# Kernel tuning notes

Measured on AMD Instinct MI355X. Metric: run time of the kernel, lower is better.

## Reference

```python
import jax, jax.numpy as jnp
import numpy as np
import math

H_HEADS = 4
SQRT_2_PI = math.sqrt(2.0 / math.pi)


def _gelu_tanh(x):
    return 0.5 * x * (1.0 + jnp.tanh(SQRT_2_PI * (x + 0.044715 * x ** 3)))


def _ln(x, g, b, eps=1e-5):
    mu = jnp.mean(x, axis=-1, keepdims=True)
    var = jnp.var(x, axis=-1, keepdims=True)
    return g * (x - mu) * jax.lax.rsqrt(var + eps) + b


def _forward(support_emb_mat, query_t, support_t, cls_embed, t_freq, t_phase,
             Wq, bq, Wk, bk, Wv, bv, Wo, bo, ln1_g, ln1_b, time_w,
             W1, b1, W2, b2, ln2_g, ln2_b, Wc, bc, bn_g, bn_b):
    B, F, MD = support_emb_mat.shape
    Q = query_t.shape[1]
    S = F + 1
    H = H_HEADS
    D = MD * H
    dph = D // H
    L = Wq.shape[0]
    BQ = B * Q

    # [CLS] + support sequence, feature-tiled to model_dim*num_heads
    cls = jnp.broadcast_to(cls_embed, (B, 1, MD))
    seq = jnp.concatenate([cls, support_emb_mat], axis=1)          # [B,S,MD]
    x = jnp.tile(seq, (1, 1, H))                                    # [B,S,D]
    x = jnp.broadcast_to(x[:, None], (B, Q, S, D)).reshape(BQ, S, D)

    # time sequence: [query_t_q, support_t...] per (b,q)
    sup = jnp.broadcast_to(support_t[:, None, :], (B, Q, F))
    t_seq = jnp.concatenate([query_t[..., None], sup], axis=-1).reshape(BQ, S)
    t_diff = t_seq[:, :, None] - t_seq[:, None, :]                  # [BQ,S,S]
    # time encoder: cos(t*freq + phase) -> [BQ,S,S,TD]
    t_emb = jnp.cos(t_diff[..., None] * t_freq + t_phase)

    # scale as in source: (dim_per_head // num_heads) ** -0.5
    scale = (dph // H) ** (-0.5)

    for l in range(L):
        bias = t_emb @ time_w[l]                                    # [BQ,S,S]
        add = jnp.tile(bias, (H, 1, 1))                             # [BQ*H,S,S]
        res = x
        # raw row-major reshape to (BQ*H, S, dph) exactly as torch .view
        q = (x @ Wq[l] + bq[l]).reshape(BQ * H, S, dph)
        k = (x @ Wk[l] + bk[l]).reshape(BQ * H, S, dph)
        v = (x @ Wv[l] + bv[l]).reshape(BQ * H, S, dph)
        attn = jax.nn.softmax(jnp.einsum('bsd,btd->bst', q, k) * scale + add, axis=-1)
        ctx = jnp.einsum('bst,btd->bsd', attn, v).reshape(BQ, S, D)
        out = _ln(res + ctx @ Wo[l] + bo[l], ln1_g[l], ln1_b[l])
        ffn = _gelu_tanh(out @ W1[l] + b1[l]) @ W2[l] + b2[l]
        x = _ln(out + ffn, ln2_g[l], ln2_b[l])

    # compress: Linear -> BatchNorm1d over seq channels (train mode) -> LeakyReLU
    h = x @ Wc + bc                                                 # [BQ,S,MD]
    mu = jnp.mean(h, axis=(0, 2), keepdims=True)
    var = jnp.var(h, axis=(0, 2), keepdims=True)
    h = bn_g[None, :, None] * (h - mu) * jax.lax.rsqrt(var + 1e-5) + bn_b[None, :, None]
    h = jnp.where(h >= 0, h, 0.01 * h)                              # LeakyReLU
    return h[:, 0, :].reshape(B, Q, MD)


def setup_inputs() -> dict:
    key = jax.random.key(0)
    ks = jax.random.split(key, 24)
    B, Q, F, MD = 128, 32, 7, 128
    H, L, FFN, TD = 4, 6, 2048, 32
    S = F + 1
    D = MD * H

    def nrm(k, shape, s=0.02):
        return jax.random.normal(k, shape, jnp.float32) * s

    inp = {
        'support_emb_mat': jax.random.normal(ks[0], (B, F, MD), jnp.float32),
        'query_t': jax.random.uniform(ks[1], (B, Q), jnp.float32) * 100.0,
        'support_t': jax.random.uniform(ks[2], (B, F), jnp.float32) * 100.0,
        'cls_embed': jax.random.uniform(ks[3], (1, MD), jnp.float32),
        't_freq': nrm(ks[4], (TD,), 1.0),
        't_phase': nrm(ks[5], (TD,), 1.0),
        'Wq': nrm(ks[6], (L, D, D)), 'bq': jnp.zeros((L, D)),
        'Wk': nrm(ks[7], (L, D, D)), 'bk': jnp.zeros((L, D)),
        'Wv': nrm(ks[8], (L, D, D)), 'bv': jnp.zeros((L, D)),
        'Wo': nrm(ks[9], (L, D, D)), 'bo': jnp.zeros((L, D)),
        'ln1_g': jnp.ones((L, D)), 'ln1_b': jnp.zeros((L, D)),
        'time_w': jnp.ones((L, TD)) * 0.001,
        'W1': nrm(ks[10], (L, D, FFN)), 'b1': jnp.zeros((L, FFN)),
        'W2': nrm(ks[11], (L, FFN, D)), 'b2': jnp.zeros((L, D)),
        'ln2_g': jnp.ones((L, D)), 'ln2_b': jnp.zeros((L, D)),
        'Wc': nrm(ks[12], (D, MD)), 'bc': jnp.zeros((MD,)),
        'bn_g': jnp.ones((S,)), 'bn_b': jnp.zeros((S,)),
    }
    return inp


def reference(support_emb_mat, query_t, support_t, cls_embed, t_freq, t_phase,
              Wq, bq, Wk, bk, Wv, bv, Wo, bo, ln1_g, ln1_b, time_w,
              W1, b1, W2, b2, ln2_g, ln2_b, Wc, bc, bn_g, bn_b):
    return _forward(support_emb_mat, query_t, support_t, cls_embed, t_freq, t_phase,
                    Wq, bq, Wk, bk, Wv, bv, Wo, bo, ln1_g, ln1_b, time_w,
                    W1, b1, W2, b2, ln2_g, ln2_b, Wc, bc, bn_g, bn_b)
```

## Files before the change

kernel.cpp:

```cpp
#include <hip/hip_runtime.h>
#include <hip/hip_bf16.h>

typedef _Float16 f16;
typedef __attribute__((ext_vector_type(8))) _Float16 f16x8;
typedef __attribute__((ext_vector_type(4))) _Float16 f16x4;
typedef __attribute__((ext_vector_type(4))) float f32x4;

#define DEVI __device__ __forceinline__

DEVI float ldf(const void* p, size_t i, int isf32) {
    if (isf32) return ((const float*)p)[i];
    unsigned int u = ((const unsigned short*)p)[i];
    union { unsigned int b; float f; } c; c.b = u << 16;
    return c.f;
}

DEVI void gld_lds16(const f16* g, f16* l) {
    __builtin_amdgcn_global_load_lds(
        (__attribute__((address_space(1))) void*)(g),
        (__attribute__((address_space(3))) void*)(l), 16, 0, 0);
}

__global__ void detect_dtype(const void* qt, int* flag) {
    if (threadIdx.x == 0 && blockIdx.x == 0) {
        const unsigned int* w = (const unsigned int*)qt;
        int cnt = 0;
        for (int i = 0; i < 64; ++i) {
            unsigned int lo = w[i] & 0xFFFFu;
            union { unsigned int b; float f; } c; c.b = lo << 16;
            if (c.f >= 1e-4f && c.f <= 100.5f) ++cnt;
        }
        *flag = (cnt >= 32) ? 0 : 1;
    }
}

__global__ __launch_bounds__(256)
void cvt_in(const void* __restrict__ src, float* __restrict__ dst, int n,
            const int* __restrict__ flag) {
    const int f32 = *flag;
    int i = blockIdx.x * 256 + threadIdx.x;
    if (i < n) dst[i] = ldf(src, i, f32);
}

__global__ __launch_bounds__(256)
void fill_out(float* out, float v) {
    out[blockIdx.x * 256 + threadIdx.x] = v;
}

template<int EPI>
__global__ __launch_bounds__(256, 4)
void gemm_bt(const f16* __restrict__ Ag, const f16* __restrict__ BTg,
             const float* __restrict__ biasg, const f16* __restrict__ resg,
             void* __restrict__ outg,
             int NT, int NTZ, int MCHUNK, int MT, int N, int K, int lda,
             long zsB, long zsBias, long zsC)
{
    const int tid  = threadIdx.x;
    const int w    = tid >> 6, lane = tid & 63;
    const int wm   = w >> 1,   wn   = w & 1;

    const int id    = blockIdx.x;
    const int pc    = MCHUNK * NTZ;
    const int chunk = id / pc;
    const int rem   = id - chunk * pc;
    const int mloc  = rem % MCHUNK;
    const int ynz   = rem / MCHUNK;
    const int z     = ynz / NT;
    const int tmB   = (chunk * MCHUNK + mloc) * (128 * MT);
    const int tn    = (ynz - z * NT) * 128;

    const f16*   BT   = BTg + (size_t)z * zsB;
    const float* bias = biasg + (size_t)z * zsBias;
    const size_t zoffC = (size_t)z * zsC;

    __shared__ __align__(16) f16 smA[2][8][64][8];
    __shared__ __align__(16) f16 smB[2][8][64][8];

    const int r16 = lane & 15, q4 = lane >> 4;
    const int iters = K >> 5;

    const f16* gA0 = Ag + (size_t)(tmB + (2 * w) * 16 + r16) * lda + q4 * 8;
    const f16* gA1 = gA0 + (size_t)16 * lda;
    const f16* gB0 = BT + (size_t)(tn + (2 * w) * 16 + r16) * K + q4 * 8;
    const f16* gB1 = gB0 + (size_t)16 * K;

    auto issue = [&](int msN, int ktN, int buf) {
        const size_t aoff = (size_t)msN * 128 * lda + (size_t)ktN * 32;
        const size_t boff = (size_t)ktN * 32;
        gld_lds16(gA0 + aoff, &smA[buf][2 * w][0][0]);
        gld_lds16(gA1 + aoff, &smA[buf][2 * w + 1][0][0]);
        gld_lds16(gB0 + boff, &smB[buf][2 * w][0][0]);
        gld_lds16(gB1 + boff, &smB[buf][2 * w + 1][0][0]);
    };

    issue(0, 0, 0);
    int stage = 0;

    for (int ms = 0; ms < MT; ++ms) {
        const int tm = tmB + ms * 128;

        f32x4 acc[4][4];
#pragma unroll
        for (int i = 0; i < 4; ++i)
#pragma unroll
            for (int j = 0; j < 4; ++j) acc[i][j] = (f32x4)0.0f;

        for (int kt = 0; kt < iters; ++kt, ++stage) {
            const int cur = stage & 1;
            __builtin_amdgcn_s_barrier();
            int ktN = kt + 1, msN = ms;
            if (ktN == iters) { ktN = 0; ++msN; }
            if (msN < MT) {
                issue(msN, ktN, cur ^ 1);
                __builtin_amdgcn_s_waitcnt(0x0F74);
            } else {
                __builtin_amdgcn_s_waitcnt(0x0F70);
            }
            __builtin_amdgcn_s_barrier();
            __asm__ __volatile__("" ::: "memory");

            f16x8 af[4], bf[4];
#pragma unroll
            for (int i = 0; i < 4; ++i) {
                af[i] = *(const f16x8*)&smA[cur][wm * 4 + i][lane][0];
                bf[i] = *(const f16x8*)&smB[cur][wn * 4 + i][lane][0];
            }
#pragma unroll
            for (int i = 0; i < 4; ++i)
#pragma unroll
                for (int j = 0; j < 4; ++j)
                    acc[i][j] = __builtin_amdgcn_mfma_f32_16x16x32_f16(
                        bf[j], af[i], acc[i][j], 0, 0, 0);
        }

        const int rowBase = tm + wm * 64;
        const int colBase = tn + wn * 64;
#pragma unroll
        for (int i = 0; i < 4; ++i) {
            const int row = rowBase + i * 16 + r16;
            const size_t rowoff = (size_t)row * N;
#pragma unroll
            for (int j = 0; j < 4; ++j) {
                const int n0 = colBase + j * 16 + q4 * 4;
                const f32x4 bv4 = *(const f32x4*)&bias[n0];
                if constexpr (EPI == 3) {
                    f32x4 o;
#pragma unroll
                    for (int r = 0; r < 4; ++r) o[r] = acc[i][j][r] + bv4[r];
                    *(f32x4*)((float*)outg + rowoff + n0) = o;
                } else {
                    f16x4 o;
#pragma unroll
                    for (int r = 0; r < 4; ++r) {
                        float v = acc[i][j][r] + bv4[r];
                        if constexpr (EPI == 2) {
                            float v2 = v * v;
                            float t  = v * (1.0f + 0.044715f * v2);
                            float e  = __expf(1.5957691216057308f * t);
                            float rc = __builtin_amdgcn_rcpf(e + 1.0f);
                            v = v - v * rc;
                        }
                        o[r] = (f16)v;
                    }
                    *(f16x4*)((f16*)outg + zoffC + rowoff + n0) = o;
                }
            }
        }
    }
}

__global__ __launch_bounds__(512, 2)
void gemm_ln(const f16* __restrict__ Ag, const f16* __restrict__ BTg,
             const float* __restrict__ bias, const f16* __restrict__ resg,
             const float* __restrict__ lng, const float* __restrict__ lnb,
             f16* __restrict__ Yg, int K, int lda)
{
    const int tid = threadIdx.x;
    const int w = tid >> 6, lane = tid & 63;
    const int wm = w >> 2, wn = w & 3;
    const int r16 = lane & 15, q4 = lane >> 4;
    const int tm = blockIdx.x * 128;

    __shared__ __align__(16) f16 smA[2][8][64][8];
    __shared__ __align__(16) f16 smB[2][32][64][8];
    __shared__ __align__(16) float lnS[128][4];
    __shared__ __align__(16) float lnQ[128][4];

    f32x4 acc[4][8];
#pragma unroll
    for (int i = 0; i < 4; ++i)
#pragma unroll
        for (int j = 0; j < 8; ++j) acc[i][j] = (f32x4)0.0f;

    const f16* gA  = Ag  + (size_t)(tm + w * 16 + r16) * lda + q4 * 8;
    const f16* gB  = BTg + (size_t)(w * 64 + r16) * K + q4 * 8;
    const int iters = K >> 5;

    auto issue = [&](int kt, int buf) {
        const size_t o = (size_t)kt * 32;
        gld_lds16(gA + o, &smA[buf][w][0][0]);
#pragma unroll
        for (int t = 0; t < 4; ++t)
            gld_lds16(gB + (size_t)(t * 16) * K + o, &smB[buf][w * 4 + t][0][0]);
    };

    issue(0, 0);
    for (int kt = 0; kt < iters; ++kt) {
        const int cur = kt & 1;
        __builtin_amdgcn_s_barrier();
        if (kt + 1 < iters) {
            issue(kt + 1, cur ^ 1);
            __builtin_amdgcn_s_waitcnt(0x0F75);
        } else {
            __builtin_amdgcn_s_waitcnt(0x0F70);
        }
        __builtin_amdgcn_s_barrier();
        __asm__ __volatile__("" ::: "memory");

        f16x8 af[4], bf[8];
#pragma unroll
        for (int i = 0; i < 4; ++i)
            af[i] = *(const f16x8*)&smA[cur][wm * 4 + i][lane][0];
#pragma unroll
        for (int j = 0; j < 8; ++j)
            bf[j] = *(const f16x8*)&smB[cur][wn * 8 + j][lane][0];
#pragma unroll
        for (int i = 0; i < 4; ++i)
#pragma unroll
            for (int j = 0; j < 8; ++j)
                acc[i][j] = __builtin_amdgcn_mfma_f32_16x16x32_f16(
                    bf[j], af[i], acc[i][j], 0, 0, 0);
    }

    const int rowB = wm * 64;
    const int colB = wn * 128;

    float ps[4], pq[4];
#pragma unroll
    for (int i = 0; i < 4; ++i) {
        const int grow = tm + rowB + i * 16 + r16;
        const size_t roff = (size_t)grow * 512;
        float s = 0.f, sq = 0.f;
#pragma unroll
        for (int j = 0; j < 8; ++j) {
            const int n0 = colB + j * 16 + q4 * 4;
            const f32x4 biv = *(const f32x4*)&bias[n0];
            const f16x4 rv  = *(const f16x4*)&resg[roff + n0];
#pragma unroll
            for (int r = 0; r < 4; ++r) {
                float v = acc[i][j][r] + biv[r] + (float)rv[r];
                acc[i][j][r] = v;
                s += v; sq += v * v;
            }
        }
        s  += __shfl_xor(s, 16, 64);  s  += __shfl_xor(s, 32, 64);
        sq += __shfl_xor(sq, 16, 64); sq += __shfl_xor(sq, 32, 64);
        ps[i] = s; pq[i] = sq;
    }
    if (q4 == 0) {
#pragma unroll
        for (int i = 0; i < 4; ++i) {
            const int lr = rowB + i * 16 + r16;
            lnS[lr][wn] = ps[i];
            lnQ[lr][wn] = pq[i];
        }
    }
    __syncthreads();

#pragma unroll
    for (int i = 0; i < 4; ++i) {
        const int lr = rowB + i * 16 + r16;
        const f32x4 s4 = *(const f32x4*)&lnS[lr][0];
        const f32x4 q4v = *(const f32x4*)&lnQ[lr][0];
        const float s  = s4[0] + s4[1] + s4[2] + s4[3];
        const float sq = q4v[0] + q4v[1] + q4v[2] + q4v[3];
        const float mu = s * (1.0f / 512.0f);
        const float var = sq * (1.0f / 512.0f) - mu * mu;
        const float rs = rsqrtf(var + 1e-5f);
        const size_t rowoff = (size_t)(tm + lr) * 512;
#pragma unroll
        for (int j = 0; j < 8; ++j) {
            const int n0 = colB + j * 16 + q4 * 4;
            const f32x4 g4 = *(const f32x4*)&lng[n0];
            const f32x4 b4 = *(const f32x4*)&lnb[n0];
            f16x4 o;
#pragma unroll
            for (int r = 0; r < 4; ++r)
                o[r] = (f16)(g4[r] * (acc[i][j][r] - mu) * rs + b4[r]);
            *(f16x4*)&Yg[rowoff + n0] = o;
        }
    }
}

__global__ __launch_bounds__(256)
void attn_kernel(const f16* __restrict__ qg, const f16* __restrict__ kg,
                 const f16* __restrict__ vg, const float* __restrict__ biasL,
                 f16* __restrict__ cg, int small)
{
    const int w = threadIdx.x >> 6, lane = threadIdx.x & 63;
    const int j = blockIdx.x * 4 + w;
    __shared__ __align__(16) f16 sQ[4][8][136];
    __shared__ __align__(16) f16 sK[4][8][136];
    __shared__ __align__(16) f16 sV[4][8][136];
    __shared__ float sP[4][8][8];

    const size_t base  = (size_t)j * 1024;
    const size_t ibase = small ? ((size_t)(j >> 7) * 4096 + (size_t)(j & 3) * 1024)
                               : base;
#pragma unroll
    for (int t = 0; t < 2; ++t) {
        int flat = (t * 64 + lane) * 8;
        int r = flat >> 7, c = flat & 127;
        *(f16x8*)&sQ[w][r][c] = *(const f16x8*)(qg + ibase + flat);
        *(f16x8*)&sK[w][r][c] = *(const f16x8*)(kg + ibase + flat);
        *(f16x8*)&sV[w][r][c] = *(const f16x8*)(vg + ibase + flat);
    }
    __syncthreads();

    const int i = lane >> 3, jj = lane & 7;
    float d = 0.f;
#pragma unroll
    for (int c = 0; c < 16; ++c) {
        f16x8 qv = *(const f16x8*)&sQ[w][i][c * 8];
        f16x8 kv = *(const f16x8*)&sK[w][jj][c * 8];
#pragma unroll
        for (int e = 0; e < 8; ++e) d += (float)qv[e] * (float)kv[e];
    }
    float s = d * 0.17677669529663687f + biasL[(size_t)(j & 4095) * 64 + lane];
    float mx = s;
    mx = fmaxf(mx, __shfl_xor(mx, 1, 64));
    mx = fmaxf(mx, __shfl_xor(mx, 2, 64));
    mx = fmaxf(mx, __shfl_xor(mx, 4, 64));
    float p = __expf(s - mx);
    float sum = p;
    sum += __shfl_xor(sum, 1, 64);
    sum += __shfl_xor(sum, 2, 64);
    sum += __shfl_xor(sum, 4, 64);
    sP[w][i][jj] = p / sum;
    __syncthreads();

#pragma unroll
    for (int t2 = 0; t2 < 8; ++t2) {
        float ap[8];
#pragma unroll
        for (int e = 0; e < 8; ++e) ap[e] = sP[w][t2][e];
#pragma unroll
        for (int h = 0; h < 2; ++h) {
            int flat = (t2 * 2 + h) * 64 + lane;
            int dd = flat & 127;
            float o = 0.f;
#pragma unroll
            for (int e = 0; e < 8; ++e) o += ap[e] * (float)sV[w][e][dd];
            cg[base + flat] = (f16)o;
        }
    }
}

__global__ __launch_bounds__(256)
void build_x0(const void* __restrict__ sup, const void* __restrict__ cls,
              f16* __restrict__ xb, const int* __restrict__ flag)
{
    const int f32 = *flag;
    const size_t idx = ((size_t)blockIdx.x * 256 + threadIdx.x) * 4;
    const int row = (int)(idx >> 9), col0 = (int)(idx & 511);
    const int s = row & 7, b = row >> 8;
    f16x4 o;
#pragma unroll
    for (int e = 0; e < 4; ++e) {
        const int md = (col0 + e) & 127;
        float v = (s == 0) ? ldf(cls, md, f32)
                           : ldf(sup, ((size_t)b * 7 + (s - 1)) * 128 + md, f32);
        o[e] = (f16)v;
    }
    *(f16x4*)(xb + idx) = o;
}

__global__ __launch_bounds__(256)
void build_x0s(const void* __restrict__ sup, const void* __restrict__ cls,
               f16* __restrict__ xs, const int* __restrict__ flag)
{
    const int f32 = *flag;
    const size_t idx = ((size_t)blockIdx.x * 256 + threadIdx.x) * 4;
    const int row = (int)(idx >> 9), col0 = (int)(idx & 511);
    const int s = row & 7, b = row >> 3;
    f16x4 o;
#pragma unroll
    for (int e = 0; e < 4; ++e) {
        const int md = (col0 + e) & 127;
        float v = (s == 0) ? ldf(cls, md, f32)
                           : ldf(sup, ((size_t)b * 7 + (s - 1)) * 128 + md, f32);
        o[e] = (f16)v;
    }
    *(f16x4*)(xs + idx) = o;
}

__global__ __launch_bounds__(256)
void bias_kernel(const void* __restrict__ qt, const void* __restrict__ st,
                 const void* __restrict__ freq, const void* __restrict__ phase,
                 const void* __restrict__ tw, float* __restrict__ biasAll,
                 const int* __restrict__ flag)
{
    const int f32 = *flag;
    const int lane = threadIdx.x & 63;
    const int bq = blockIdx.x * 4 + (threadIdx.x >> 6);
    const int b = bq >> 5, qq = bq & 31;
    const int i = lane >> 3, jj = lane & 7;
    const float ti = (i  == 0) ? ldf(qt, b * 32 + qq, f32) : ldf(st, b * 7 + i  - 1, f32);
    const float tj = (jj == 0) ? ldf(qt, b * 32 + qq, f32) : ldf(st, b * 7 + jj - 1, f32);
    const float td = ti - tj;
    float a[6] = {0.f, 0.f, 0.f, 0.f, 0.f, 0.f};
    for (int t = 0; t < 32; ++t) {
        float c = __cosf(td * ldf(freq, t, f32) + ldf(phase, t, f32));
#pragma unroll
        for (int l = 0; l < 6; ++l) a[l] += c * ldf(tw, l * 32 + t, f32);
    }
#pragma unroll
    for (int l = 0; l < 6; ++l)
        biasAll[(size_t)l * (4096 * 64) + (size_t)bq * 64 + lane] = a[l];
}

__global__ __launch_bounds__(256)
void transpose_cvt(const void* __restrict__ W, f16* __restrict__ WT,
                   int K, int N, long zsW, long zsWT, const int* __restrict__ flag)
{
    const int f32 = *flag;
    const size_t zoff = (size_t)blockIdx.z * zsW;
    f16* WTz = WT + (size_t)blockIdx.z * zsWT;
    __shared__ float tile[64][65];
    const int tn = blockIdx.x * 64, tk = blockIdx.y * 64;
#pragma unroll
    for (int t = 0; t < 16; ++t) {
        int idx = t * 256 + threadIdx.x;
        int r = idx >> 6, c = idx & 63;
        tile[r][c] = ldf(W, zoff + (size_t)(tk + r) * N + tn + c, f32);
    }
    __syncthreads();
#pragma unroll
    for (int t = 0; t < 16; ++t) {
        int idx = t * 256 + threadIdx.x;
        int r = idx >> 6, c = idx & 63;
        WTz[(size_t)(tn + r) * K + tk + c] = (f16)tile[c][r];
    }
}

__global__ __launch_bounds__(256)
void gather_qkvb(const void* __restrict__ bq, const void* __restrict__ bk,
                 const void* __restrict__ bv, float* __restrict__ dst,
                 const int* __restrict__ flag)
{
    const int f32 = *flag;
    int i = blockIdx.x * 256 + threadIdx.x;
    if (i < 9216) {
        int z = i / 3072, rem = i % 3072;
        const void* src = (z == 0) ? bq : ((z == 1) ? bk : bv);
        dst[i] = ldf(src, rem, f32);
    }
}

__global__ __launch_bounds__(256)
void bn_reduce(const float* __restrict__ h0, float* __restrict__ stats)
{
    const int t = blockIdx.x * 256 + threadIdx.x;
    float s = 0.f, ss = 0.f;
#pragma unroll
    for (int k = 0; k < 8; ++k) {
        float v = h0[t + k * 65536];
        s += v; ss += v * v;
    }
#pragma unroll
    for (int m = 1; m <= 32; m <<= 1) {
        s  += __shfl_xor(s, m, 64);
        ss += __shfl_xor(ss, m, 64);
    }
    __shared__ float ls[8];
    const int w = threadIdx.x >> 6, lane = threadIdx.x & 63;
    if (lane == 0) { ls[w] = s; ls[4 + w] = ss; }
    __syncthreads();
    if (threadIdx.x == 0) {
        atomicAdd(&stats[0], ls[0] + ls[1] + ls[2] + ls[3]);
        atomicAdd(&stats[1], ls[4] + ls[5] + ls[6] + ls[7]);
    }
}

__global__ __launch_bounds__(256)
void bn_apply(const float* __restrict__ h0, const float* __restrict__ stats,
              const float* __restrict__ bnp, float* __restrict__ out)
{
    const int t = blockIdx.x * 256 + threadIdx.x;
    const float mu  = stats[0] * (1.0f / 524288.0f);
    const float var = stats[1] * (1.0f / 524288.0f) - mu * mu;
    const float rs  = rsqrtf(var + 1e-5f);
    float v = bnp[0] * (h0[t] - mu) * rs + bnp[8];
    v = (v >= 0.f) ? v : 0.01f * v;
    out[t] = v;
}

extern "C" void kernel_launch(void* const* d_in, const int* in_sizes, int n_in,
                              void* d_out, int out_size, void* d_ws, size_t ws_size,
                              hipStream_t stream)
{
    (void)in_sizes; (void)n_in; (void)out_size;
    const void* sup   = d_in[0];
    const void* qt    = d_in[1];
    const void* st    = d_in[2];
    const void* cls   = d_in[3];
    const void* freq  = d_in[4];
    const void* phase = d_in[5];
    const void* Wq = d_in[6];  const void* bqv = d_in[7];
    const void* Wk = d_in[8];  const void* bkv = d_in[9];
    const void* Wv = d_in[10]; const void* bvv = d_in[11];
    const void* Wo = d_in[12]; const void* bo  = d_in[13];
    const void* ln1g = d_in[14]; const void* ln1b = d_in[15];
    const void* tw = d_in[16];
    const void* W1 = d_in[17]; const void* b1 = d_in[18];
    const void* W2 = d_in[19]; const void* b2 = d_in[20];
    const void* ln2g = d_in[21]; const void* ln2b = d_in[22];
    const void* Wc = d_in[23]; const void* bc = d_in[24];
    const void* bng = d_in[25]; const void* bnb = d_in[26];

    const size_t NEEDED = 245658240;
    if (ws_size < NEEDED) {
        fill_out<<<2048, 256, 0, stream>>>((float*)d_out, 999.0f);
        return;
    }

    char* ws = (char*)d_ws;
    f16*   wt      = (f16*)(ws + 0);
    float* biasAll = (float*)(ws + 37879808);
    float* qkvb    = (float*)(ws + 44171264);
    float* prm     = (float*)(ws + 44208128);
    float* stats   = (float*)(ws + 44331584);
    int*   flag    = (int*)  (ws + 44331592);
    f16*   xb      = (f16*)(ws + 44331648);
    f16*   ob      = (f16*)(ws + 77886080);
    char*  region  = ws + 111440512;
    f16*   qb      = (f16*)(region);
    f16*   kb      = (f16*)(region + 33554432);
    f16*   vb      = (f16*)(region + 67108864);
    f16*   cb      = (f16*)(region + 100663296);
    f16*   qs      = (f16*)(region);
    f16*   xs      = (f16*)(region + 100663296);
    f16*   fbuf    = (f16*)(region);
    float* h0      = (float*)(region);

    detect_dtype<<<1, 64, 0, stream>>>(qt, flag);

    cvt_in<<<12, 256, 0, stream>>>(bo,   prm + 0,     3072,  flag);
    cvt_in<<<48, 256, 0, stream>>>(b1,   prm + 3072,  12288, flag);
    cvt_in<<<12, 256, 0, stream>>>(b2,   prm + 15360, 3072,  flag);
    cvt_in<<<1,  256, 0, stream>>>(bc,   prm + 18432, 128,   flag);
    cvt_in<<<12, 256, 0, stream>>>(ln1g, prm + 18560, 3072,  flag);
    cvt_in<<<12, 256, 0, stream>>>(ln1b, prm + 21632, 3072,  flag);
    cvt_in<<<12, 256, 0, stream>>>(ln2g, prm + 24704, 3072,  flag);
    cvt_in<<<12, 256, 0, stream>>>(ln2b, prm + 27776, 3072,  flag);
    cvt_in<<<1,  256, 0, stream>>>(bng,  prm + 30848, 8,     flag);
    cvt_in<<<1,  256, 0, stream>>>(bnb,  prm + 30856, 8,     flag);

    transpose_cvt<<<dim3(8, 8, 6),  256, 0, stream>>>(Wq, wt + 0,        512, 512,  262144, 262144, flag);
    transpose_cvt<<<dim3(8, 8, 6),  256, 0, stream>>>(Wk, wt + 1572864,  512, 512,  262144, 262144, flag);
    transpose_cvt<<<dim3(8, 8, 6),  256, 0, stream>>>(Wv, wt + 3145728,  512, 512,  262144, 262144, flag);
    transpose_cvt<<<dim3(8, 8, 6),  256, 0, stream>>>(Wo, wt + 4718592,  512, 512,  262144, 262144, flag);
    transpose_cvt<<<dim3(32, 8, 6), 256, 0, stream>>>(W1, wt + 6291456,  512, 2048, 1048576, 1048576, flag);
    transpose_cvt<<<dim3(8, 32, 6), 256, 0, stream>>>(W2, wt + 12582912, 2048, 512, 1048576, 1048576, flag);
    transpose_cvt<<<dim3(2, 8, 1),  256, 0, stream>>>(Wc, wt + 18874368, 512, 128,  0, 0, flag);
    gather_qkvb<<<36, 256, 0, stream>>>(bqv, bkv, bvv, qkvb, flag);
    build_x0<<<16384, 256, 0, stream>>>(sup, cls, xb, flag);
    build_x0s<<<512, 256, 0, stream>>>(sup, cls, xs, flag);
    bias_kernel<<<1024, 256, 0, stream>>>(qt, st, freq, phase, tw, biasAll, flag);
    hipMemsetAsync(stats, 0, 8, stream);

    for (int l = 0; l < 6; ++l) {
        if (l == 0) {
            gemm_bt<0><<<96, 256, 0, stream>>>(
                xs, wt, qkvb, nullptr, qs,
                4, 12, 8, 1, 512, 512, 512, 1572864, 3072, 524288);
            attn_kernel<<<4096, 256, 0, stream>>>(
                qs, qs + 524288, qs + 1048576, biasAll, cb, 1);
        } else {
            gemm_bt<0><<<1536, 256, 0, stream>>>(
                xb, wt + l * 262144, qkvb + l * 512, nullptr, qb,
                4, 12, 32, 2, 512, 512, 512, 1572864, 3072, 16777216);
            attn_kernel<<<4096, 256, 0, stream>>>(
                qb, kb, vb, biasAll + (size_t)l * 262144, cb, 0);
        }
        gemm_ln<<<256, 512, 0, stream>>>(
            cb, wt + 4718592 + l * 262144, prm + 0 + l * 512, xb,
            prm + 18560 + l * 512, prm + 21632 + l * 512, ob, 512, 512);
        gemm_bt<2><<<2048, 256, 0, stream>>>(
            ob, wt + 6291456 + l * 1048576, prm + 3072 + l * 2048, nullptr, fbuf,
            16, 16, 32, 2, 2048, 512, 512, 0, 0, 0);
        gemm_ln<<<256, 512, 0, stream>>>(
            fbuf, wt + 12582912 + l * 1048576, prm + 15360 + l * 512, ob,
            prm + 24704 + l * 512, prm + 27776 + l * 512, xb, 2048, 2048);
    }

    gemm_bt<3><<<32, 256, 0, stream>>>(
        xb, wt + 18874368, prm + 18432, nullptr, h0,
        1, 1, 32, 1, 128, 512, 4096 , 0, 0, 0);
    bn_reduce<<<256, 256, 0, stream>>>(h0, stats);
    bn_apply<<<2048, 256, 0, stream>>>(h0, stats, prm + 30848, (float*)d_out);
}
```

Measured before the change: 2.911 ms.

## Add 256x256-tile GEMM kernel for QKV and FFN1 projections

Introduces a new 512-thread GEMM with 256x256 output tiles, a 64-wide K step, double-buffered global-to-LDS loads, and an XCD-aware block remapping. It replaces the older gemm_bt for the QKV projections and the GELU FFN-up projection. Larger tiles raise arithmetic intensity and cut redundant operand loads. The cost is higher register and LDS pressure (128 accumulator floats per thread) and fewer blocks, especially the 24-block layer-0 launch.

New measurement: 2.876 ms. About the same (-1.2%).

```diff
diff --git a/kernel.cpp b/kernel.cpp
--- a/kernel.cpp
+++ b/kernel.cpp
@@ -45,6 +45,122 @@
 __global__ __launch_bounds__(256)
 void fill_out(float* out, float v) {
     out[blockIdx.x * 256 + threadIdx.x] = v;
+}
+
+template<int EPI>
+__global__ __launch_bounds__(512, 2)
+void gemm256(const f16* __restrict__ Ag, const f16* __restrict__ BTg,
+             const float* __restrict__ biasg, void* __restrict__ outg,
+             int gridM, int gridN, int N, int K, int lda,
+             long zsB, long zsBias, long zsC)
+{
+    const int tid = threadIdx.x;
+    const int w = tid >> 6, lane = tid & 63;
+    const int wm = w >> 2, wn = w & 3;
+    const int r16 = lane & 15, q4 = lane >> 4;
+
+    const int cpx = gridDim.x >> 3;
+    const int id  = (blockIdx.x & 7) * cpx + (blockIdx.x >> 3);
+
+    const int mloc = id % gridM;
+    const int ynz  = id / gridM;
+    const int z    = ynz / gridN;
+    const int nt   = ynz - z * gridN;
+    const int tm = mloc * 256, tn = nt * 256;
+
+    const f16*   BT   = BTg + (size_t)z * zsB;
+    const float* bias = biasg + (size_t)z * zsBias;
+    const size_t zoffC = (size_t)z * zsC;
+
+    __shared__ __align__(16) f16 smA[2][2][16][64][8];
+    __shared__ __align__(16) f16 smB[2][2][16][64][8];
+
+    const f16* gA[4]; const f16* gB[4];
+#pragma unroll
+    for (int t = 0; t < 4; ++t) {
+        const int c = 4 * w + t, kk = c >> 4, rc = c & 15;
+        gA[t] = Ag + (size_t)(tm + rc * 16 + r16) * lda + kk * 32 + q4 * 8;
+        gB[t] = BT + (size_t)(tn + rc * 16 + r16) * K  + kk * 32 + q4 * 8;
+    }
+    f16* const smAbase = &smA[0][0][0][0][0];
+    f16* const smBbase = &smB[0][0][0][0][0];
+    const int coff = (4 * w) * 512;
+
+    auto issue = [&](int kt, int buf) {
+        const size_t o = (size_t)kt * 64;
+        const int bo = buf * 16384 + coff;
+#pragma unroll
+        for (int t = 0; t < 4; ++t) {
+            gld_lds16(gA[t] + o, smAbase + bo + t * 512);
+            gld_lds16(gB[t] + o, smBbase + bo + t * 512);
+        }
+    };
+
+    f32x4 acc[8][4];
+#pragma unroll
+    for (int i = 0; i < 8; ++i)
+#pragma unroll
+        for (int j = 0; j < 4; ++j) acc[i][j] = (f32x4)0.0f;
+
+    const int iters = K >> 6;
+    issue(0, 0);
+    __builtin_amdgcn_s_waitcnt(0x0F70);
+    __builtin_amdgcn_s_barrier();
+    __asm__ __volatile__("" ::: "memory");
+
+    for (int kt = 0; kt < iters; ++kt) {
+        const int cur = kt & 1;
+        const bool more = (kt + 1 < iters);
+        if (more) issue(kt + 1, cur ^ 1);
+#pragma unroll
+        for (int kk = 0; kk < 2; ++kk) {
+            f16x8 af[8], bf[4];
+#pragma unroll
+            for (int i = 0; i < 8; ++i)
+                af[i] = *(const f16x8*)&smA[cur][kk][wm * 8 + i][lane][0];
+#pragma unroll
+            for (int j = 0; j < 4; ++j)
+                bf[j] = *(const f16x8*)&smB[cur][kk][wn * 4 + j][lane][0];
+#pragma unroll
+            for (int i = 0; i < 8; ++i)
+#pragma unroll
+                for (int j = 0; j < 4; ++j)
+                    acc[i][j] = __builtin_amdgcn_mfma_f32_16x16x32_f16(
+                        bf[j], af[i], acc[i][j], 0, 0, 0);
+        }
+        if (more) {
+            __builtin_amdgcn_s_waitcnt(0x0F70);
+            __builtin_amdgcn_s_barrier();
+            __asm__ __volatile__("" ::: "memory");
+        }
+    }
+
+    const int rowBase = tm + wm * 128;
+    const int colBase = tn + wn * 64;
+#pragma unroll
+    for (int i = 0; i < 8; ++i) {
+        const int row = rowBase + i * 16 + r16;
+        const size_t rowoff = (size_t)row * N;
+#pragma unroll
+        for (int j = 0; j < 4; ++j) {
+            const int n0 = colBase + j * 16 + q4 * 4;
+            const f32x4 bv4 = *(const f32x4*)&bias[n0];
+            f16x4 o;
+#pragma unroll
+            for (int r = 0; r < 4; ++r) {
+                float v = acc[i][j][r] + bv4[r];
+                if constexpr (EPI == 2) {
+                    float v2 = v * v;
+                    float t  = v * (1.0f + 0.044715f * v2);
+                    float e  = __expf(1.5957691216057308f * t);
+                    float rc = __builtin_amdgcn_rcpf(e + 1.0f);
+                    v = v - v * rc;
+                }
+                o[r] = (f16)v;
+            }
+            *(f16x4*)((f16*)outg + zoffC + rowoff + n0) = o;
+        }
+    }
 }
 
 template<int EPI>
@@ -571,24 +687,24 @@
 
     for (int l = 0; l < 6; ++l) {
         if (l == 0) {
-            gemm_bt<0><<<96, 256, 0, stream>>>(
-                xs, wt, qkvb, nullptr, qs,
-                4, 12, 8, 1, 512, 512, 512, 1572864, 3072, 524288);
+            gemm256<0><<<24, 512, 0, stream>>>(
+                xs, wt, qkvb, qs,
+                4, 2, 512, 512, 512, 1572864, 3072, 524288);
             attn_kernel<<<4096, 256, 0, stream>>>(
                 qs, qs + 524288, qs + 1048576, biasAll, cb, 1);
         } else {
-            gemm_bt<0><<<1536, 256, 0, stream>>>(
-                xb, wt + l * 262144, qkvb + l * 512, nullptr, qb,
-                4, 12, 32, 2, 512, 512, 512, 1572864, 3072, 16777216);
+            gemm256<0><<<768, 512, 0, stream>>>(
+                xb, wt + l * 262144, qkvb + l * 512, qb,
+                128, 2, 512, 512, 512, 1572864, 3072, 16777216);
             attn_kernel<<<4096, 256, 0, stream>>>(
                 qb, kb, vb, biasAll + (size_t)l * 262144, cb, 0);
         }
         gemm_ln<<<256, 512, 0, stream>>>(
             cb, wt + 4718592 + l * 262144, prm + 0 + l * 512, xb,
             prm + 18560 + l * 512, prm + 21632 + l * 512, ob, 512, 512);
-        gemm_bt<2><<<2048, 256, 0, stream>>>(
-            ob, wt + 6291456 + l * 1048576, prm + 3072 + l * 2048, nullptr, fbuf,
-            16, 16, 32, 2, 2048, 512, 512, 0, 0, 0);
+        gemm256<2><<<1024, 512, 0, stream>>>(
+            ob, wt + 6291456 + l * 1048576, prm + 3072 + l * 2048, fbuf,
+            128, 8, 2048, 512, 512, 0, 0, 0);
         gemm_ln<<<256, 512, 0, stream>>>(
             fbuf, wt + 12582912 + l * 1048576, prm + 15360 + l * 512, ob,
             prm + 24704 + l * 512, prm + 27776 + l * 512, xb, 2048, 2048);
```

## Compute last-layer FFN only for CLS rows and simplify GEMM tiling

Applied to the files above, without the earlier changes.

Replaces the multi-M-tile gemm_bt with a simpler one-tile-per-block kernel that uses an XCD-aware block index swizzle. It also restricts the final layer's FFN and its LayerNorm to only the rows the classifier reads (stride 4096, i.e. the CLS rows), which drops most of the last FFN's work. The cost is more blocks, with the prologue repeated per tile, and no cross-M-tile prefetch.

After: 2.830 ms. -2.8%, faster.

```diff
diff --git a/kernel.cpp b/kernel.cpp
--- a/kernel.cpp
+++ b/kernel.cpp
@@ -49,25 +49,24 @@
 
 template<int EPI>
 __global__ __launch_bounds__(256, 4)
-void gemm_bt(const f16* __restrict__ Ag, const f16* __restrict__ BTg,
-             const float* __restrict__ biasg, const f16* __restrict__ resg,
-             void* __restrict__ outg,
-             int NT, int NTZ, int MCHUNK, int MT, int N, int K, int lda,
-             long zsB, long zsBias, long zsC)
+void gemm_bt2(const f16* __restrict__ Ag, const f16* __restrict__ BTg,
+              const float* __restrict__ biasg, void* __restrict__ outg,
+              int NZ, int gridN, int N, int K, int lda,
+              long zsB, long zsBias, long zsC)
 {
     const int tid  = threadIdx.x;
     const int w    = tid >> 6, lane = tid & 63;
     const int wm   = w >> 1,   wn   = w & 1;
-
-    const int id    = blockIdx.x;
-    const int pc    = MCHUNK * NTZ;
-    const int chunk = id / pc;
-    const int rem   = id - chunk * pc;
-    const int mloc  = rem % MCHUNK;
-    const int ynz   = rem / MCHUNK;
-    const int z     = ynz / NT;
-    const int tmB   = (chunk * MCHUNK + mloc) * (128 * MT);
-    const int tn    = (ynz - z * NT) * 128;
+    const int r16  = lane & 15, q4 = lane >> 4;
+
+    const int cpx = gridDim.x >> 3;
+    const int id  = (blockIdx.x & 7) * cpx + (blockIdx.x >> 3);
+
+    const int nz   = id % NZ;
+    const int mloc = id / NZ;
+    const int z    = nz / gridN;
+    const int nt   = nz - z * gridN;
+    const int tm   = mloc * 128, tn = nt * 128;
 
     const f16*   BT   = BTg + (size_t)z * zsB;
     const float* bias = biasg + (size_t)z * zsBias;
@@ -76,94 +75,84 @@
     __shared__ __align__(16) f16 smA[2][8][64][8];
     __shared__ __align__(16) f16 smB[2][8][64][8];
 
-    const int r16 = lane & 15, q4 = lane >> 4;
     const int iters = K >> 5;
 
-    const f16* gA0 = Ag + (size_t)(tmB + (2 * w) * 16 + r16) * lda + q4 * 8;
+    const f16* gA0 = Ag + (size_t)(tm + (2 * w) * 16 + r16) * lda + q4 * 8;
     const f16* gA1 = gA0 + (size_t)16 * lda;
     const f16* gB0 = BT + (size_t)(tn + (2 * w) * 16 + r16) * K + q4 * 8;
     const f16* gB1 = gB0 + (size_t)16 * K;
 
-    auto issue = [&](int msN, int ktN, int buf) {
-        const size_t aoff = (size_t)msN * 128 * lda + (size_t)ktN * 32;
-        const size_t boff = (size_t)ktN * 32;
-        gld_lds16(gA0 + aoff, &smA[buf][2 * w][0][0]);
-        gld_lds16(gA1 + aoff, &smA[buf][2 * w + 1][0][0]);
-        gld_lds16(gB0 + boff, &smB[buf][2 * w][0][0]);
-        gld_lds16(gB1 + boff, &smB[buf][2 * w + 1][0][0]);
+    auto issue = [&](int kt, int buf) {
+        const size_t o = (size_t)kt * 32;
+        gld_lds16(gA0 + o, &smA[buf][2 * w][0][0]);
+        gld_lds16(gA1 + o, &smA[buf][2 * w + 1][0][0]);
+        gld_lds16(gB0 + o, &smB[buf][2 * w][0][0]);
+        gld_lds16(gB1 + o, &smB[buf][2 * w + 1][0][0]);
     };
 
-    issue(0, 0, 0);
-    int stage = 0;
-
-    for (int ms = 0; ms < MT; ++ms) {
-        const int tm = tmB + ms * 128;
-
-        f32x4 acc[4][4];
+    f32x4 acc[4][4];
+#pragma unroll
+    for (int i = 0; i < 4; ++i)
+#pragma unroll
+        for (int j = 0; j < 4; ++j) acc[i][j] = (f32x4)0.0f;
+
+    issue(0, 0);
+    for (int kt = 0; kt < iters; ++kt) {
+        const int cur = kt & 1;
+        __builtin_amdgcn_s_barrier();
+        if (kt + 1 < iters) {
+            issue(kt + 1, cur ^ 1);
+            __builtin_amdgcn_s_waitcnt(0x0F74);
+        } else {
+            __builtin_amdgcn_s_waitcnt(0x0F70);
+        }
+        __builtin_amdgcn_s_barrier();
+        __asm__ __volatile__("" ::: "memory");
+
+        f16x8 af[4], bf[4];
+#pragma unroll
+        for (int i = 0; i < 4; ++i) {
+            af[i] = *(const f16x8*)&smA[cur][wm * 4 + i][lane][0];
+            bf[i] = *(const f16x8*)&smB[cur][wn * 4 + i][lane][0];
+        }
 #pragma unroll
         for (int i = 0; i < 4; ++i)
 #pragma unroll
-            for (int j = 0; j < 4; ++j) acc[i][j] = (f32x4)0.0f;
-
-        for (int kt = 0; kt < iters; ++kt, ++stage) {
-            const int cur = stage & 1;
-            __builtin_amdgcn_s_barrier();
-            int ktN = kt + 1, msN = ms;
-            if (ktN == iters) { ktN = 0; ++msN; }
-            if (msN < MT) {
-                issue(msN, ktN, cur ^ 1);
-                __builtin_amdgcn_s_waitcnt(0x0F74);
+            for (int j = 0; j < 4; ++j)
+                acc[i][j] = __builtin_amdgcn_mfma_f32_16x16x32_f16(
+                    bf[j], af[i], acc[i][j], 0, 0, 0);
+    }
+
+    const int rowBase = tm + wm * 64;
+    const int colBase = tn + wn * 64;
+#pragma unroll
+    for (int i = 0; i < 4; ++i) {
+        const int row = rowBase + i * 16 + r16;
+        const size_t rowoff = (size_t)row * N;
+#pragma unroll
+        for (int j = 0; j < 4; ++j) {
+            const int n0 = colBase + j * 16 + q4 * 4;
+            const f32x4 bv4 = *(const f32x4*)&bias[n0];
+            if constexpr (EPI == 3) {
+                f32x4 o;
+#pragma unroll
+                for (int r = 0; r < 4; ++r) o[r] = acc[i][j][r] + bv4[r];
+                *(f32x4*)((float*)outg + rowoff + n0) = o;
             } else {
-                __builtin_amdgcn_s_waitcnt(0x0F70);
-            }
-            __builtin_amdgcn_s_barrier();
-            __asm__ __volatile__("" ::: "memory");
-
-            f16x8 af[4], bf[4];
-#pragma unroll
-            for (int i = 0; i < 4; ++i) {
-                af[i] = *(const f16x8*)&smA[cur][wm * 4 + i][lane][0];
-                bf[i] = *(const f16x8*)&smB[cur][wn * 4 + i][lane][0];
-            }
-#pragma unroll
-            for (int i = 0; i < 4; ++i)
-#pragma unroll
-                for (int j = 0; j < 4; ++j)
-                    acc[i][j] = __builtin_amdgcn_mfma_f32_16x16x32_f16(
-                        bf[j], af[i], acc[i][j], 0, 0, 0);
-        }
-
-        const int rowBase = tm + wm * 64;
-        const int colBase = tn + wn * 64;
-#pragma unroll
-        for (int i = 0; i < 4; ++i) {
-            const int row = rowBase + i * 16 + r16;
-            const size_t rowoff = (size_t)row * N;
-#pragma unroll
-            for (int j = 0; j < 4; ++j) {
-                const int n0 = colBase + j * 16 + q4 * 4;
-                const f32x4 bv4 = *(const f32x4*)&bias[n0];
-                if constexpr (EPI == 3) {
-                    f32x4 o;
-#pragma unroll
-                    for (int r = 0; r < 4; ++r) o[r] = acc[i][j][r] + bv4[r];
-                    *(f32x4*)((float*)outg + rowoff + n0) = o;
-                } else {
-                    f16x4 o;
-#pragma unroll
-                    for (int r = 0; r < 4; ++r) {
-                        float v = acc[i][j][r] + bv4[r];
-                        if constexpr (EPI == 2) {
-                            float v2 = v * v;
-                            float t  = v * (1.0f + 0.044715f * v2);
-                            float e  = __expf(1.5957691216057308f * t);
-                            float rc = __builtin_amdgcn_rcpf(e + 1.0f);
-                            v = v - v * rc;
-                        }
-                        o[r] = (f16)v;
+                f16x4 o;
+#pragma unroll
+                for (int r = 0; r < 4; ++r) {
+                    float v = acc[i][j][r] + bv4[r];
+                    if constexpr (EPI == 2) {
+                        float v2 = v * v;
+                        float t  = v * (1.0f + 0.044715f * v2);
+                        float e  = __expf(1.5957691216057308f * t);
+                        float rc = __builtin_amdgcn_rcpf(e + 1.0f);
+                        v = v - v * rc;
                     }
-                    *(f16x4*)((f16*)outg + zoffC + rowoff + n0) = o;
+                    o[r] = (f16)v;
                 }
+                *(f16x4*)((f16*)outg + zoffC + rowoff + n0) = o;
             }
         }
     }
@@ -173,7 +162,7 @@
 void gemm_ln(const f16* __restrict__ Ag, const f16* __restrict__ BTg,
              const float* __restrict__ bias, const f16* __restrict__ resg,
              const float* __restrict__ lng, const float* __restrict__ lnb,
-             f16* __restrict__ Yg, int K, int lda)
+             f16* __restrict__ Yg, int K, int lda, int rstride)
 {
     const int tid = threadIdx.x;
     const int w = tid >> 6, lane = tid & 63;
@@ -239,7 +228,7 @@
 #pragma unroll
     for (int i = 0; i < 4; ++i) {
         const int grow = tm + rowB + i * 16 + r16;
-        const size_t roff = (size_t)grow * 512;
+        const size_t roff = (size_t)grow * rstride;
         float s = 0.f, sq = 0.f;
 #pragma unroll
         for (int j = 0; j < 8; ++j) {
@@ -571,32 +560,41 @@
 
     for (int l = 0; l < 6; ++l) {
         if (l == 0) {
-            gemm_bt<0><<<96, 256, 0, stream>>>(
-                xs, wt, qkvb, nullptr, qs,
-                4, 12, 8, 1, 512, 512, 512, 1572864, 3072, 524288);
+            gemm_bt2<0><<<96, 256, 0, stream>>>(
+                xs, wt, qkvb, qs,
+                12, 4, 512, 512, 512, 1572864, 3072, 524288);
             attn_kernel<<<4096, 256, 0, stream>>>(
                 qs, qs + 524288, qs + 1048576, biasAll, cb, 1);
         } else {
-            gemm_bt<0><<<1536, 256, 0, stream>>>(
-                xb, wt + l * 262144, qkvb + l * 512, nullptr, qb,
-                4, 12, 32, 2, 512, 512, 512, 1572864, 3072, 16777216);
+            gemm_bt2<0><<<3072, 256, 0, stream>>>(
+                xb, wt + l * 262144, qkvb + l * 512, qb,
+                12, 4, 512, 512, 512, 1572864, 3072, 16777216);
             attn_kernel<<<4096, 256, 0, stream>>>(
                 qb, kb, vb, biasAll + (size_t)l * 262144, cb, 0);
         }
         gemm_ln<<<256, 512, 0, stream>>>(
             cb, wt + 4718592 + l * 262144, prm + 0 + l * 512, xb,
-            prm + 18560 + l * 512, prm + 21632 + l * 512, ob, 512, 512);
-        gemm_bt<2><<<2048, 256, 0, stream>>>(
-            ob, wt + 6291456 + l * 1048576, prm + 3072 + l * 2048, nullptr, fbuf,
-            16, 16, 32, 2, 2048, 512, 512, 0, 0, 0);
-        gemm_ln<<<256, 512, 0, stream>>>(
-            fbuf, wt + 12582912 + l * 1048576, prm + 15360 + l * 512, ob,
-            prm + 24704 + l * 512, prm + 27776 + l * 512, xb, 2048, 2048);
-    }
-
-    gemm_bt<3><<<32, 256, 0, stream>>>(
-        xb, wt + 18874368, prm + 18432, nullptr, h0,
-        1, 1, 32, 1, 128, 512, 4096 , 0, 0, 0);
+            prm + 18560 + l * 512, prm + 21632 + l * 512, ob, 512, 512, 512);
+        if (l < 5) {
+            gemm_bt2<2><<<4096, 256, 0, stream>>>(
+                ob, wt + 6291456 + l * 1048576, prm + 3072 + l * 2048, fbuf,
+                16, 16, 2048, 512, 512, 0, 0, 0);
+            gemm_ln<<<256, 512, 0, stream>>>(
+                fbuf, wt + 12582912 + l * 1048576, prm + 15360 + l * 512, ob,
+                prm + 24704 + l * 512, prm + 27776 + l * 512, xb, 2048, 2048, 512);
+        } else {
+            gemm_bt2<2><<<512, 256, 0, stream>>>(
+                ob, wt + 6291456 + l * 1048576, prm + 3072 + l * 2048, fbuf,
+                16, 16, 2048, 512, 4096, 0, 0, 0);
+            gemm_ln<<<32, 512, 0, stream>>>(
+                fbuf, wt + 12582912 + l * 1048576, prm + 15360 + l * 512, ob,
+                prm + 24704 + l * 512, prm + 27776 + l * 512, cb, 2048, 2048, 4096);
+        }
+    }
+
+    gemm_bt2<3><<<32, 256, 0, stream>>>(
+        cb, wt + 18874368, prm + 18432, h0,
+        1, 1, 128, 512, 512, 0, 0, 0);
     bn_reduce<<<256, 256, 0, stream>>>(h0, stats);
     bn_apply<<<2048, 256, 0, stream>>>(h0, stats, prm + 30848, (float*)d_out);
 }
```
